# Performance work log

Hardware: AMD Instinct MI355X
Metric: run time of the kernel (lower is better)

The kernel has to match this reference:

```python
import jax, jax.numpy as jnp
import numpy as np

B, LE, LS, DE, DS = 16, 1024, 1024, 1024, 1024


def setup_inputs() -> dict:
    key = jax.random.key(0)
    k1, k2, k3 = jax.random.split(key, 3)
    edit_encodings = jax.random.normal(k1, (B, LE, DE), dtype=jnp.float32)
    src_encodings = jax.random.normal(k2, (B, LS, DS), dtype=jnp.float32)
    # torch nn.Linear(DE, DS, bias=False) weight has shape (DS, DE)
    W = jax.random.normal(k3, (DS, DE), dtype=jnp.float32) * (1.0 / np.sqrt(DE))
    # padding masks: 1 for padding. Per-example valid lengths in [L/2, L].
    edit_lens = np.linspace(LE // 2, LE, B).astype(np.int32)
    src_lens = np.linspace(LS, LS // 2, B).astype(np.int32)
    edit_sent_masks = (np.arange(LE)[None, :] >= edit_lens[:, None]).astype(np.int32)
    src_sent_masks = (np.arange(LS)[None, :] >= src_lens[:, None]).astype(np.int32)
    return {
        "edit_encodings": edit_encodings,
        "src_encodings": src_encodings,
        "edit_sent_masks": jnp.asarray(edit_sent_masks),
        "src_sent_masks": jnp.asarray(src_sent_masks),
        "W": W,
    }


def reference(edit_encodings, src_encodings, edit_sent_masks, src_sent_masks, W):
    # sim: (B, LE, LS) = (edit @ W^T) @ src^T
    proj = jnp.einsum('bed,sd->bes', edit_encodings, W)          # (B, LE, DS)
    sim = jnp.einsum('bes,bls->bel', proj, src_encodings)        # (B, LE, LS)
    neg_inf = jnp.float32(-jnp.inf)
    edit_sim = jnp.where(src_sent_masks[:, None, :].astype(bool), neg_inf, sim)
    src_sim = jnp.where(edit_sent_masks[:, :, None].astype(bool), neg_inf, sim)
    edit_weights = jax.nn.softmax(edit_sim, axis=-1)             # over src positions
    src_weights = jax.nn.softmax(src_sim, axis=1)                # over edit positions
    edit_ctx = jnp.einsum('bel,bls->bes', edit_weights, src_encodings)  # (B, LE, DS)
    src_ctx = jnp.einsum('bel,bed->bld', src_weights, edit_encodings)   # (B, LS, DE)
    return (edit_ctx, src_ctx)
```

## Files before the change

### kernel.cpp

```cpp
#include <hip/hip_runtime.h>
#include <math.h>

#define BATCH 16

typedef __attribute__((ext_vector_type(8))) short s16x8;
typedef __attribute__((ext_vector_type(8))) unsigned short u16x8;
typedef __attribute__((ext_vector_type(4))) float f32x4;

__device__ inline unsigned short f2bf_rn(float f) {
  unsigned u = __float_as_uint(f);
  u += 0x7FFF + ((u >> 16) & 1);
  return (unsigned short)(u >> 16);
}
__device__ inline float bf2f(unsigned short h) {
  return __uint_as_float(((unsigned)h) << 16);
}

__device__ __forceinline__ void gload16(const unsigned short* g, unsigned short* l) {
  __builtin_amdgcn_global_load_lds(
      (__attribute__((address_space(1))) void*)g,
      (__attribute__((address_space(3))) void*)l, 16, 0, 0);
}

__global__ __launch_bounds__(256) void cvt_split3(
    const float* __restrict__ X0, unsigned short* __restrict__ H0,
    unsigned short* __restrict__ L0, const float* __restrict__ X1,
    unsigned short* __restrict__ H1, unsigned short* __restrict__ L1,
    const float* __restrict__ X2, unsigned short* __restrict__ H2,
    unsigned short* __restrict__ L2) {
  const int bid = blockIdx.x;
  const float* X;
  unsigned short *H, *L;
  size_t base;
  if (bid < 16384) { X = X0; H = H0; L = L0; base = (size_t)bid << 8; }
  else if (bid < 32768) { X = X1; H = H1; L = L1; base = (size_t)(bid - 16384) << 8; }
  else { X = X2; H = H2; L = L2; base = (size_t)(bid - 32768) << 8; }
  const size_t i = (base + threadIdx.x) << 2;
  f32x4 v = *(const f32x4*)(X + i);
  ushort4 h, l;
  h.x = f2bf_rn(v[0]); l.x = f2bf_rn(v[0] - bf2f(h.x));
  h.y = f2bf_rn(v[1]); l.y = f2bf_rn(v[1] - bf2f(h.y));
  h.z = f2bf_rn(v[2]); l.z = f2bf_rn(v[2] - bf2f(h.z));
  h.w = f2bf_rn(v[3]); l.w = f2bf_rn(v[3] - bf2f(h.w));
  *(ushort4*)(H + i) = h;
  *(ushort4*)(L + i) = l;
}

template <int HILO, int SPLIT_OUT>
__global__ __launch_bounds__(512, 2) void gemm8p(
    const unsigned short* __restrict__ AH, const unsigned short* __restrict__ AL,
    const unsigned short* __restrict__ BH, const unsigned short* __restrict__ BL,
    void* __restrict__ Cout, void* __restrict__ CoutL,
    long long sA, long long sB, long long sC, int batched) {
  constexpr int NARR = HILO ? 4 : 2;
  __shared__ __align__(16) unsigned short lds[2][NARR][8192];
  const int tid = threadIdx.x;
  const int wg = ((blockIdx.x & 7) << 5) | (blockIdx.x >> 3);
  int z, bm, bn;
  if (batched) {
    z = wg >> 4; bm = ((wg >> 2) & 3) << 8; bn = (wg & 3) << 8;
  } else {
    z = 0; bm = (wg >> 2) << 8; bn = (wg & 3) << 8;
  }
  const int wave = tid >> 6, lane = tid & 63;
  const int wm = wave >> 2, wn = wave & 3;
  const int fr = lane & 15, fks = lane >> 4;

  const int svrow = tid >> 2;
  const int scol = ((tid & 3) ^ ((tid >> 3) & 3)) << 3;
  const unsigned short* gA0 = AH + (size_t)z * sA + (size_t)(bm + svrow) * 1024 + scol;
  const unsigned short* gB0 = BH + (size_t)z * sB + (size_t)(bn + svrow) * 1024 + scol;
  const unsigned short* gA1 = HILO ? (AL + (size_t)z * sA + (size_t)(bm + svrow) * 1024 + scol) : gA0;
  const unsigned short* gB1 = HILO ? (BL + (size_t)z * sB + (size_t)(bn + svrow) * 1024 + scol) : gB0;
  const int lwb = wave << 9;

  int aoff[8], boff[4];
#pragma unroll
  for (int m = 0; m < 8; m++) {
    const int r = (wm << 7) + (m << 4) + fr;
    aoff[m] = (r << 5) + ((fks ^ ((r >> 1) & 3)) << 3);
  }
#pragma unroll
  for (int n = 0; n < 4; n++) {
    const int r = (wn << 6) + (n << 4) + fr;
    boff[n] = (r << 5) + ((fks ^ ((r >> 1) & 3)) << 3);
  }

  f32x4 acc[8][4];
#pragma unroll
  for (int m = 0; m < 8; m++)
#pragma unroll
    for (int n = 0; n < 4; n++) acc[m][n] = (f32x4)(0.f);

#define ISS(NXT, ARR, G, Q, KO) \
  gload16((G) + ((size_t)(Q) << 17) + (KO), &lds[NXT][ARR][((Q) << 12) + lwb])

  ISS(0, 0, gA0, 0, 0); ISS(0, 0, gA0, 1, 0);
  ISS(0, 1, gB0, 0, 0); ISS(0, 1, gB0, 1, 0);
  if (HILO) {
    ISS(0, 2, gA1, 0, 0); ISS(0, 2, gA1, 1, 0);
    ISS(0, 3, gB1, 0, 0); ISS(0, 3, gB1, 1, 0);
  }
  __syncthreads();

#pragma unroll 1
  for (int kt = 0; kt < 32; ++kt) {
    const int cur = kt & 1, nxt = cur ^ 1;
    const int kn = (kt + 1) << 5;
    const bool pf = kt < 31;
    const unsigned short* LAH = lds[cur][0];
    const unsigned short* LBH = lds[cur][1];
    const unsigned short* LAL = lds[cur][HILO ? 2 : 0];
    const unsigned short* LBL = lds[cur][HILO ? 3 : 1];
    s16x8 ah[4], al[4], bh[4], bl[4];

#define LDA4(QM)                                                         \
  do {                                                                   \
    _Pragma("unroll") for (int m_ = 0; m_ < 4; m_++) {                   \
      const int o_ = aoff[((QM) << 2) + m_];                             \
      ah[m_] = *(const s16x8*)&LAH[o_];                                  \
      if (HILO) al[m_] = *(const s16x8*)&LAL[o_];                        \
    }                                                                    \
  } while (0)
#define LDBALL()                                                         \
  do {                                                                   \
    _Pragma("unroll") for (int n_ = 0; n_ < 4; n_++) {                   \
      const int o_ = boff[n_];                                           \
      bh[n_] = *(const s16x8*)&LBH[o_];                                  \
      if (HILO) bl[n_] = *(const s16x8*)&LBL[o_];                        \
    }                                                                    \
  } while (0)
#define MMQ(QM)                                                                  \
  do {                                                                           \
    if (HILO) {                                                                  \
      _Pragma("unroll") for (int m_ = 0; m_ < 4; m_++)                           \
          _Pragma("unroll") for (int n_ = 0; n_ < 4; n_++)                       \
              acc[((QM) << 2) + m_][n_] =                                        \
          __builtin_amdgcn_mfma_f32_16x16x32_bf16(al[m_], bh[n_],                \
                                                  acc[((QM) << 2) + m_][n_], 0, 0, 0); \
      _Pragma("unroll") for (int m_ = 0; m_ < 4; m_++)                           \
          _Pragma("unroll") for (int n_ = 0; n_ < 4; n_++)                       \
              acc[((QM) << 2) + m_][n_] =                                        \
          __builtin_amdgcn_mfma_f32_16x16x32_bf16(ah[m_], bl[n_],                \
                                                  acc[((QM) << 2) + m_][n_], 0, 0, 0); \
    }                                                                            \
    _Pragma("unroll") for (int m_ = 0; m_ < 4; m_++)                             \
        _Pragma("unroll") for (int n_ = 0; n_ < 4; n_++)                         \
            acc[((QM) << 2) + m_][n_] =                                          \
        __builtin_amdgcn_mfma_f32_16x16x32_bf16(ah[m_], bh[n_],                  \
                                                acc[((QM) << 2) + m_][n_], 0, 0, 0);   \
  } while (0)

    LDA4(0); LDBALL();
    if (pf) {
      ISS(nxt, 0, gA0, 0, kn); ISS(nxt, 0, gA0, 1, kn);
      ISS(nxt, 1, gB0, 0, kn); ISS(nxt, 1, gB0, 1, kn);
      if (HILO) {
        ISS(nxt, 2, gA1, 0, kn); ISS(nxt, 2, gA1, 1, kn);
        ISS(nxt, 3, gB1, 0, kn); ISS(nxt, 3, gB1, 1, kn);
      }
    }
    __builtin_amdgcn_s_barrier();
    __builtin_amdgcn_s_setprio(1); MMQ(0); __builtin_amdgcn_s_setprio(0);
    __builtin_amdgcn_s_barrier();

    LDA4(1);
    __builtin_amdgcn_s_barrier();
    __builtin_amdgcn_s_setprio(1); MMQ(1); __builtin_amdgcn_s_setprio(0);
    __syncthreads();
#undef LDA4
#undef LDBALL
#undef MMQ
  }
#undef ISS

  const int cr = (lane >> 4) << 2;
  const int crow0 = bm + (wm << 7);
  const int ccol0 = bn + (wn << 6);
  if (SPLIT_OUT) {
    unsigned short* CH = (unsigned short*)Cout + (size_t)z * sC;
    unsigned short* CL = (unsigned short*)CoutL + (size_t)z * sC;
#pragma unroll
    for (int m = 0; m < 8; m++)
#pragma unroll
      for (int r = 0; r < 4; r++) {
        const size_t base = (size_t)(crow0 + (m << 4) + cr + r) * 1024 + ccol0 + fr;
#pragma unroll
        for (int n = 0; n < 4; n++) {
          float f = acc[m][n][r];
          unsigned short h = f2bf_rn(f);
          CH[base + (n << 4)] = h;
          CL[base + (n << 4)] = f2bf_rn(f - bf2f(h));
        }
      }
  } else {
    float* C = (float*)Cout + (size_t)z * sC;
#pragma unroll
    for (int m = 0; m < 8; m++)
#pragma unroll
      for (int r = 0; r < 4; r++) {
        float* cp = C + (size_t)(crow0 + (m << 4) + cr + r) * 1024 + ccol0 + fr;
#pragma unroll
        for (int n = 0; n < 4; n++) cp[n << 4] = acc[m][n][r];
      }
  }
}

__device__ inline float waveMax(float v) {
#pragma unroll
  for (int o = 32; o > 0; o >>= 1) v = fmaxf(v, __shfl_down(v, o, 64));
  return v;
}
__device__ inline float waveSum(float v) {
#pragma unroll
  for (int o = 32; o > 0; o >>= 1) v += __shfl_down(v, o, 64);
  return v;
}

__global__ __launch_bounds__(256) void row_softmax_kernel(
    const float* __restrict__ sim, const int* __restrict__ smask,
    unsigned short* __restrict__ out) {
  const int row = blockIdx.x;
  const int b = row >> 10;
  const float* x = sim + ((size_t)row << 10);
  const int* mk = smask + (b << 10);
  const int t = threadIdx.x;

  float4 v = ((const float4*)x)[t];
  int4 m = ((const int4*)mk)[t];
  float vv[4] = {v.x, v.y, v.z, v.w};
  const int mmv[4] = {m.x, m.y, m.z, m.w};

  float mx = -3.0e38f;
#pragma unroll
  for (int i = 0; i < 4; i++)
    if (!mmv[i]) mx = fmaxf(mx, vv[i]);

  __shared__ float red[4];
  float wmx = waveMax(mx);
  const int wave = t >> 6;
  if ((t & 63) == 0) red[wave] = wmx;
  __syncthreads();
  mx = fmaxf(fmaxf(red[0], red[1]), fmaxf(red[2], red[3]));
  __syncthreads();

  float s = 0.f;
#pragma unroll
  for (int i = 0; i < 4; i++) {
    float e = mmv[i] ? 0.f : __expf(vv[i] - mx);
    vv[i] = e;
    s += e;
  }
  float ws = waveSum(s);
  if ((t & 63) == 0) red[wave] = ws;
  __syncthreads();
  s = red[0] + red[1] + red[2] + red[3];
  float inv = 1.0f / s;

  ushort4 o;
  o.x = f2bf_rn(vv[0] * inv);
  o.y = f2bf_rn(vv[1] * inv);
  o.z = f2bf_rn(vv[2] * inv);
  o.w = f2bf_rn(vv[3] * inv);
  *(ushort4*)&out[((size_t)row << 10) + (t << 2)] = o;
}

__global__ __launch_bounds__(256) void col_partial(
    const float* __restrict__ sim, const int* __restrict__ emask,
    float* __restrict__ pmax, float* __restrict__ psum) {
  const int b = blockIdx.z;
  const int ec = blockIdx.y;
  const int l = (blockIdx.x << 8) + threadIdx.x;
  const float* p = sim + ((size_t)b << 20) + (((size_t)ec << 6) << 10) + l;
  const int* mk = emask + (b << 10) + (ec << 6);
  float mx0 = -1.0e30f, s0 = 0.f, mx1 = -1.0e30f, s1 = 0.f;
#pragma unroll 4
  for (int i = 0; i < 64; i += 2) {
    float v0 = mk[i] ? -3.0e38f : p[(size_t)i << 10];
    float v1 = mk[i + 1] ? -3.0e38f : p[(size_t)(i + 1) << 10];
    float n0 = fmaxf(mx0, v0);
    s0 = s0 * __expf(mx0 - n0) + __expf(v0 - n0);
    mx0 = n0;
    float n1 = fmaxf(mx1, v1);
    s1 = s1 * __expf(mx1 - n1) + __expf(v1 - n1);
    mx1 = n1;
  }
  float M = fmaxf(mx0, mx1);
  float S = s0 * __expf(mx0 - M) + s1 * __expf(mx1 - M);
  const int o = (((b << 4) + ec) << 10) + l;
  pmax[o] = M;
  psum[o] = S;
}

__global__ __launch_bounds__(256) void col_weights_T(
    const float* __restrict__ sim, const int* __restrict__ emask,
    const float* __restrict__ pmax, const float* __restrict__ psum,
    unsigned short* __restrict__ wT) {
  const int b = blockIdx.z;
  const int l0 = blockIdx.x << 6;
  const int e0 = blockIdx.y << 6;
  const int t = threadIdx.x;
  __shared__ float Ml[64], Il[64];
  __shared__ int msk[64];
  __shared__ float gm[4][64], gs[4][64];
  __shared__ unsigned short tile[64][72];

  {
    const int ll = t & 63, g = t >> 6;
    float m = -1.0e30f, s = 0.f;
#pragma unroll
    for (int q = 0; q < 4; q++) {
      int ec = g + (q << 2);
      const int o = (((b << 4) + ec) << 10) + l0 + ll;
      float pm = pmax[o], ps = psum[o];
      float nm = fmaxf(m, pm);
      s = s * __expf(m - nm) + ps * __expf(pm - nm);
      m = nm;
    }
    gm[g][ll] = m;
    gs[g][ll] = s;
    __syncthreads();
    if (t < 64) {
      float M = fmaxf(fmaxf(gm[0][t], gm[1][t]), fmaxf(gm[2][t], gm[3][t]));
      float S = 0.f;
#pragma unroll
      for (int q = 0; q < 4; q++) S += gs[q][t] * __expf(gm[q][t] - M);
      Ml[t] = M;
      Il[t] = 1.0f / S;
      msk[t] = emask[(b << 10) + e0 + t];
    }
    __syncthreads();
  }

  const int lane = t & 63, wv = t >> 6;
#pragma unroll
  for (int i = 0; i < 16; i++) {
    const int el = (wv << 4) + i;
    float v = sim[((size_t)b << 20) + ((size_t)(e0 + el) << 10) + l0 + lane];
    float w = msk[el] ? 0.f : __expf(v - Ml[lane]) * Il[lane];
    tile[lane][el] = f2bf_rn(w);
  }
  __syncthreads();
  const int r = t >> 2, seg = (t & 3) << 4;
  u16x8 v0 = *(const u16x8*)&tile[r][seg];
  u16x8 v1 = *(const u16x8*)&tile[r][seg + 8];
  size_t o = ((size_t)((b << 10) + l0 + r) << 10) + e0 + seg;
  *(u16x8*)&wT[o] = v0;
  *(u16x8*)&wT[o + 8] = v1;
}

__global__ __launch_bounds__(256) void transpose16(
    const unsigned short* __restrict__ X, unsigned short* __restrict__ XT) {
  __shared__ unsigned short ts[64][72];
  const int b = blockIdx.z;
  const int d0 = blockIdx.x << 6, l0 = blockIdx.y << 6;
  const int t = threadIdx.x;
  const unsigned short* Xb = X + ((size_t)b << 20);
  unsigned short* Tb = XT + ((size_t)b << 20);
  const int row = t >> 2, seg = (t & 3) << 4;
  u16x8 v0 = *(const u16x8*)&Xb[((size_t)(l0 + row) << 10) + d0 + seg];
  u16x8 v1 = *(const u16x8*)&Xb[((size_t)(l0 + row) << 10) + d0 + seg + 8];
#pragma unroll
  for (int i = 0; i < 8; i++) ts[seg + i][row] = v0[i];
#pragma unroll
  for (int i = 0; i < 8; i++) ts[seg + 8 + i][row] = v1[i];
  __syncthreads();
  u16x8 o0 = *(const u16x8*)&ts[row][seg];
  u16x8 o1 = *(const u16x8*)&ts[row][seg + 8];
  size_t o = ((size_t)(d0 + row) << 10) + l0 + seg;
  *(u16x8*)&Tb[o] = o0;
  *(u16x8*)&Tb[o + 8] = o1;
}

extern "C" void kernel_launch(void* const* d_in, const int* in_sizes, int n_in,
                              void* d_out, int out_size, void* d_ws,
                              size_t ws_size, hipStream_t stream) {
  const float* edit = (const float*)d_in[0];
  const float* src = (const float*)d_in[1];
  const int* emask = (const int*)d_in[2];
  const int* smask = (const int*)d_in[3];
  const float* W = (const float*)d_in[4];

  char* ws = (char*)d_ws;
  char* dob = (char*)d_out;

  unsigned short* eH = (unsigned short*)ws;
  unsigned short* sH = (unsigned short*)(ws + ((size_t)32 << 20));
  unsigned short* pH = (unsigned short*)(ws + ((size_t)64 << 20));
  unsigned short* pL = (unsigned short*)(ws + ((size_t)96 << 20));
  unsigned short* wE = pH;
  unsigned short* wST = pL;
  unsigned short* editT = sH;

  unsigned short* eL = (unsigned short*)dob;
  unsigned short* sL = (unsigned short*)(dob + ((size_t)64 << 20));
  unsigned short* WH = (unsigned short*)(dob + ((size_t)96 << 20));
  unsigned short* WL = (unsigned short*)(dob + ((size_t)98 << 20));
  float* sim = (float*)dob;
  float* pmax = (float*)(dob + ((size_t)64 << 20));
  float* psum = (float*)(dob + ((size_t)65 << 20));
  unsigned short* srcT = (unsigned short*)(dob + ((size_t)64 << 20));
  float* out_edit = (float*)dob;
  float* out_src = (float*)(dob + ((size_t)64 << 20));

  const long long S1 = 1LL << 20;
  dim3 blk(256), blk512(512);

  cvt_split3<<<dim3(33792), blk, 0, stream>>>(edit, eH, eL, src, sH, sL, W, WH, WL);

  gemm8p<1, 1><<<dim3(256), blk512, 0, stream>>>(
      eH, eL, WH, WL, (void*)pH, (void*)pL, 0, 0, 0, 0);

  gemm8p<1, 0><<<dim3(256), blk512, 0, stream>>>(
      pH, pL, sH, sL, (void*)sim, nullptr, S1, S1, S1, 1);

  row_softmax_kernel<<<dim3(BATCH << 10), blk, 0, stream>>>(sim, smask, wE);
  col_partial<<<dim3(4, 16, BATCH), blk, 0, stream>>>(sim, emask, pmax, psum);
  col_weights_T<<<dim3(16, 16, BATCH), blk, 0, stream>>>(sim, emask, pmax, psum, wST);

  transpose16<<<dim3(16, 16, BATCH), blk, 0, stream>>>(sH, srcT);
  transpose16<<<dim3(16, 16, BATCH), blk, 0, stream>>>(eH, editT);

  gemm8p<0, 0><<<dim3(256), blk512, 0, stream>>>(
      wE, nullptr, srcT, nullptr, (void*)out_edit, nullptr, S1, S1, S1, 1);
  gemm8p<0, 0><<<dim3(256), blk512, 0, stream>>>(
      wST, nullptr, editT, nullptr, (void*)out_src, nullptr, S1, S1, S1, 1);
}
```

Before: 551.1 us.

## Prefetch two K-tiles ahead with vmcnt waits instead of full syncthreads

The GEMM main loop now issues global-to-LDS loads two stages ahead, into the buffer just consumed, and waits on them with explicit vmcnt counters rather than draining all outstanding memory operations through __syncthreads each iteration. The second half's LDS reads finish before a barrier, and only then is the next stage refilled into the current buffer, overlapping those loads with the second MFMA batch. The aim is to hide global-load latency better and cut barrier stalls. Correctness depends on the hand-tuned vmcnt values matching the number of outstanding loads per stage.

```diff
diff --git a/kernel.cpp b/kernel.cpp
--- a/kernel.cpp
+++ b/kernel.cpp
@@ -92,22 +92,24 @@
 #pragma unroll
     for (int n = 0; n < 4; n++) acc[m][n] = (f32x4)(0.f);
 
-#define ISS(NXT, ARR, G, Q, KO) \
-  gload16((G) + ((size_t)(Q) << 17) + (KO), &lds[NXT][ARR][((Q) << 12) + lwb])
-
-  ISS(0, 0, gA0, 0, 0); ISS(0, 0, gA0, 1, 0);
-  ISS(0, 1, gB0, 0, 0); ISS(0, 1, gB0, 1, 0);
-  if (HILO) {
-    ISS(0, 2, gA1, 0, 0); ISS(0, 2, gA1, 1, 0);
-    ISS(0, 3, gB1, 0, 0); ISS(0, 3, gB1, 1, 0);
-  }
-  __syncthreads();
+#define ISS(BUF, ARR, G, Q, KO) \
+  gload16((G) + ((size_t)(Q) << 17) + (KO), &lds[BUF][ARR][((Q) << 12) + lwb])
+#define STAGE(BUF, KO)                                  \
+  do {                                                  \
+    ISS(BUF, 0, gA0, 0, KO); ISS(BUF, 0, gA0, 1, KO);   \
+    ISS(BUF, 1, gB0, 0, KO); ISS(BUF, 1, gB0, 1, KO);   \
+    if (HILO) {                                         \
+      ISS(BUF, 2, gA1, 0, KO); ISS(BUF, 2, gA1, 1, KO); \
+      ISS(BUF, 3, gB1, 0, KO); ISS(BUF, 3, gB1, 1, KO); \
+    }                                                   \
+  } while (0)
+
+  STAGE(0, 0);
+  STAGE(1, 32);
 
 #pragma unroll 1
   for (int kt = 0; kt < 32; ++kt) {
-    const int cur = kt & 1, nxt = cur ^ 1;
-    const int kn = (kt + 1) << 5;
-    const bool pf = kt < 31;
+    const int cur = kt & 1;
     const unsigned short* LAH = lds[cur][0];
     const unsigned short* LBH = lds[cur][1];
     const unsigned short* LAL = lds[cur][HILO ? 2 : 0];
@@ -151,28 +153,29 @@
                                                 acc[((QM) << 2) + m_][n_], 0, 0, 0);   \
   } while (0)
 
-    LDA4(0); LDBALL();
-    if (pf) {
-      ISS(nxt, 0, gA0, 0, kn); ISS(nxt, 0, gA0, 1, kn);
-      ISS(nxt, 1, gB0, 0, kn); ISS(nxt, 1, gB0, 1, kn);
-      if (HILO) {
-        ISS(nxt, 2, gA1, 0, kn); ISS(nxt, 2, gA1, 1, kn);
-        ISS(nxt, 3, gB1, 0, kn); ISS(nxt, 3, gB1, 1, kn);
-      }
+    if (kt < 31) {
+      if (HILO) asm volatile("s_waitcnt vmcnt(8)" ::: "memory");
+      else      asm volatile("s_waitcnt vmcnt(4)" ::: "memory");
+    } else {
+      asm volatile("s_waitcnt vmcnt(0)" ::: "memory");
     }
     __builtin_amdgcn_s_barrier();
+
+    LDA4(0); LDBALL();
     __builtin_amdgcn_s_setprio(1); MMQ(0); __builtin_amdgcn_s_setprio(0);
+
+    LDA4(1);
+    asm volatile("s_waitcnt lgkmcnt(0)" ::: "memory");
+    __builtin_amdgcn_sched_barrier(0);
     __builtin_amdgcn_s_barrier();
-
-    LDA4(1);
-    __builtin_amdgcn_s_barrier();
+    if (kt < 30) STAGE(cur, (kt + 2) << 5);
     __builtin_amdgcn_s_setprio(1); MMQ(1); __builtin_amdgcn_s_setprio(0);
-    __syncthreads();
 #undef LDA4
 #undef LDBALL
 #undef MMQ
   }
 #undef ISS
+#undef STAGE
 
   const int cr = (lane >> 4) << 2;
   const int crow0 = bm + (wm << 7);
```

Result: no change. 548.8 us (-0.4%).
